# Kernel tuning notes

Hardware: AMD Instinct MI355X
Metric: run time of the kernel (lower is better)

The kernel has to match this reference:

```python
import jax, jax.numpy as jnp
import numpy as np

K_STEPS = 10
ALPHA = 0.1


def setup_inputs() -> dict:
    key = jax.random.key(0)
    k0, k1, k2, k3 = jax.random.split(key, 4)
    N, E, C_IN, C_HID, C_OUT = 100000, 3200000, 512, 256, 64
    x = jax.random.normal(k0, (N, C_IN), dtype=jnp.float32)
    edge_index = jax.random.randint(k1, (2, E), 0, N, dtype=jnp.int64)
    W1 = jax.random.normal(k2, (C_IN, C_HID), dtype=jnp.float32) * (1.0 / np.sqrt(C_IN))
    b1 = jnp.zeros((C_HID,), dtype=jnp.float32)
    W2 = jax.random.normal(k3, (C_HID, C_OUT), dtype=jnp.float32) * (1.0 / np.sqrt(C_HID))
    b2 = jnp.zeros((C_OUT,), dtype=jnp.float32)
    return {"x": x, "edge_index": edge_index, "W1": W1, "b1": b1, "W2": W2, "b2": b2}


def reference(x, edge_index, W1, b1, W2, b2):
    N = x.shape[0]
    src, dst = edge_index[0], edge_index[1]
    # add self-loops (PyG APPNP default)
    loop = jnp.arange(N, dtype=src.dtype)
    src = jnp.concatenate([src, loop])
    dst = jnp.concatenate([dst, loop])
    # GCN symmetric normalization: D^{-1/2} A D^{-1/2}
    deg = jax.ops.segment_sum(jnp.ones_like(dst, dtype=x.dtype), dst, num_segments=N)
    dinv = jnp.where(deg > 0, deg ** -0.5, jnp.zeros_like(deg))
    norm = dinv[src] * dinv[dst]  # [E+N]
    # MLP (dropout is identity at inference)
    h = jax.nn.relu(x @ W1 + b1) @ W2 + b2  # [N, C_OUT]
    # K-step APPNP propagation with teleport
    out = h
    for _ in range(K_STEPS):
        msg = norm[:, None] * out[src]  # [E+N, C_OUT]
        agg = jax.ops.segment_sum(msg, dst, num_segments=N)
        out = (1.0 - ALPHA) * agg + ALPHA * h
    return jax.nn.log_softmax(out, axis=1)
```

## Files before the change

### kernel.cpp

```cpp
#include <hip/hip_runtime.h>
#include <hip/hip_bf16.h>

#define C_IN  512
#define C_HID 256
#define C_OUT 64
#define K_STEPS 10
#define ALPHA 0.1f

#define BKT_SHIFT 9
#define BKT_NODES 512
#define BCAP 24576
#define EPB 4096

typedef _Float16 half8 __attribute__((ext_vector_type(8)));
typedef float f32x4 __attribute__((ext_vector_type(4)));


__global__ __launch_bounds__(256) void k_bucketA(
    const int* __restrict__ src, const int* __restrict__ dst, int E,
    int* __restrict__ bcursor, long long* __restrict__ bedges, int nbkt)
{
    __shared__ int lcount[256];
    __shared__ int lbase[256];
    int t = threadIdx.x;
    int base = blockIdx.x * EPB;
    for (int i = t; i < nbkt; i += 256) lcount[i] = 0;
    __syncthreads();

    int       mybkt[16];
    int       myoff[16];
    long long mypk[16];
    #pragma unroll
    for (int j = 0; j < 16; j++) {
        int e = base + j * 256 + t;
        if (e < E) {
            int s = src[e], d = dst[e];
            int b = d >> BKT_SHIFT;
            mybkt[j] = b;
            mypk[j]  = ((long long)d << 32) | (unsigned int)s;
            myoff[j] = atomicAdd(&lcount[b], 1);
        } else {
            mybkt[j] = -1;
        }
    }
    __syncthreads();
    for (int i = t; i < nbkt; i += 256)
        lbase[i] = lcount[i] ? atomicAdd(&bcursor[i], lcount[i]) : 0;
    __syncthreads();
    #pragma unroll
    for (int j = 0; j < 16; j++) {
        if (mybkt[j] >= 0) {
            int p = lbase[mybkt[j]] + myoff[j];
            bedges[(size_t)mybkt[j] * BCAP + p] = mypk[j];
        }
    }
}

__global__ __launch_bounds__(256) void k_bcount(
    const int* __restrict__ bcursor, const long long* __restrict__ bedges,
    int* __restrict__ counts, int N)
{
    __shared__ int lcnt[BKT_NODES];
    int b = blockIdx.x, t = threadIdx.x;
    int nodebase = b << BKT_SHIFT;
    for (int i = t; i < BKT_NODES; i += 256) lcnt[i] = 0;
    __syncthreads();
    int cnt = bcursor[b];
    const long long* be = bedges + (size_t)b * BCAP;
    for (int i = t; i < cnt; i += 256) {
        int d = (int)(be[i] >> 32);
        atomicAdd(&lcnt[d - nodebase], 1);
    }
    __syncthreads();
    for (int i = t; i < BKT_NODES; i += 256) {
        int node = nodebase + i;
        if (node < N) counts[node] = lcnt[i];
    }
}

__global__ __launch_bounds__(256) void k_bscatter(
    const int* __restrict__ bcursor, const long long* __restrict__ bedges,
    const int* __restrict__ rowptr, int* __restrict__ csr_src, int N)
{
    __shared__ int lcur[BKT_NODES];
    int b = blockIdx.x, t = threadIdx.x;
    int nodebase = b << BKT_SHIFT;
    for (int i = t; i < BKT_NODES; i += 256) {
        int node = nodebase + i;
        lcur[i] = (node < N) ? rowptr[node] : 0;
    }
    __syncthreads();
    int cnt = bcursor[b];
    const long long* be = bedges + (size_t)b * BCAP;
    for (int i = t; i < cnt; i += 256) {
        long long pk = be[i];
        int d = (int)(pk >> 32);
        int s = (int)pk;
        int p = atomicAdd(&lcur[d - nodebase], 1);
        csr_src[p] = s;
    }
}


__global__ void k_dinv(const int* __restrict__ counts, float* __restrict__ dinv, int N) {
    int i = blockIdx.x * blockDim.x + threadIdx.x;
    if (i < N) {
        float deg = (float)(counts[i] + 1);
        dinv[i] = 1.0f / sqrtf(deg);
    }
}

#define SCAN_CHUNK 2048

__global__ void k_scan1(const int* __restrict__ counts, int N, int* __restrict__ bsum) {
    __shared__ int sdata[256];
    int b = blockIdx.x, t = threadIdx.x;
    int base = b * SCAN_CHUNK;
    int sum = 0;
    for (int i = t; i < SCAN_CHUNK; i += 256) {
        int idx = base + i;
        sum += (idx < N) ? counts[idx] : 0;
    }
    sdata[t] = sum;
    __syncthreads();
    for (int off = 128; off; off >>= 1) {
        if (t < off) sdata[t] += sdata[t + off];
        __syncthreads();
    }
    if (t == 0) bsum[b] = sdata[0];
}

__global__ void k_scan2(int* __restrict__ bsum, int nb, int E, int* __restrict__ rowptr, int N) {
    if (blockIdx.x == 0 && threadIdx.x == 0) {
        int run = 0;
        for (int i = 0; i < nb; i++) { int v = bsum[i]; bsum[i] = run; run += v; }
        rowptr[N] = E;
    }
}

__global__ void k_scan3(const int* __restrict__ counts, int N,
                        const int* __restrict__ bsum, int* __restrict__ rowptr) {
    __shared__ int sdata[256];
    int b = blockIdx.x, t = threadIdx.x;
    int base = b * SCAN_CHUNK;
    int vals[8];
    int local = 0;
    #pragma unroll
    for (int i = 0; i < 8; i++) {
        int idx = base + t * 8 + i;
        vals[i] = (idx < N) ? counts[idx] : 0;
        local += vals[i];
    }
    sdata[t] = local;
    __syncthreads();
    for (int off = 1; off < 256; off <<= 1) {
        int y = 0;
        if (t >= off) y = sdata[t - off];
        __syncthreads();
        sdata[t] += y;
        __syncthreads();
    }
    int excl = (t == 0) ? 0 : sdata[t - 1];
    int run = bsum[b] + excl;
    #pragma unroll
    for (int i = 0; i < 8; i++) {
        int idx = base + t * 8 + i;
        if (idx < N) rowptr[idx] = run;
        run += vals[i];
    }
}


__global__ void k_w1t(const float* __restrict__ W, _Float16* __restrict__ Wt) {
    int i = blockIdx.x * 256 + threadIdx.x;
    int k = i >> 8, n = i & 255;
    Wt[(size_t)n * 512 + k] = (_Float16)W[i];
}

__global__ void k_w2t(const float* __restrict__ W, _Float16* __restrict__ Wt) {
    int i = blockIdx.x * 256 + threadIdx.x;
    int k = i >> 6, n = i & 63;
    Wt[(size_t)n * 256 + k] = (_Float16)W[i];
}


__global__ __launch_bounds__(128, 2) void k_mlp1(
    const float* __restrict__ A, const _Float16* __restrict__ Bt,
    const float* __restrict__ bias, _Float16* __restrict__ C, int M)
{
    __shared__ float lds[3][64 * 32];

    int t    = threadIdx.x;
    int lane = t & 63;
    int wc   = t >> 6;
    int bm   = blockIdx.x * 64;
    int mrow = lane & 15;
    int kg   = lane >> 4;

    int srow = t >> 3;
    int cgs  = (t & 7) ^ ((t >> 3) & 7);

    const float* gsrc[4];
    #pragma unroll
    for (int q = 0; q < 4; q++) {
        int gr = bm + q * 16 + srow;
        if (gr >= M) gr = M - 1;
        gsrc[q] = A + (size_t)gr * 512 + cgs * 4;
    }

    #define STAGE(buf, ks)                                                       \
        {                                                                        \
            _Pragma("unroll")                                                    \
            for (int q = 0; q < 4; q++) {                                        \
                __builtin_amdgcn_global_load_lds(                                \
                    (const __attribute__((address_space(1))) void*)(gsrc[q] + (ks) * 32), \
                    (__attribute__((address_space(3))) void*)((char*)&lds[buf][0] + q * 2048 + t * 16), \
                    16, 0, 0);                                                   \
            }                                                                    \
        }

    f32x4 acc[4][8] = {};

    int m7 = lane & 7;
    int rbase[4];
    #pragma unroll
    for (int mi = 0; mi < 4; mi++)
        rbase[mi] = (mi * 16 + mrow) * 32;
    int p0 = ((2 * kg) ^ m7) * 4;
    int p1 = ((2 * kg + 1) ^ m7) * 4;

    STAGE(0, 0);
    STAGE(1, 1);

    #pragma unroll
    for (int ks = 0; ks < 16; ks++) {
        asm volatile("s_waitcnt vmcnt(4) lgkmcnt(0)" ::: "memory");
        __builtin_amdgcn_s_barrier();

        half8 b[8];
        #pragma unroll
        for (int ni = 0; ni < 8; ni++) {
            int n = wc * 128 + ni * 16 + mrow;
            b[ni] = *(const half8*)(Bt + (size_t)n * 512 + ks * 32 + kg * 8);
        }

        if (ks < 14) STAGE((ks + 2) % 3, ks + 2);

        const float* lbuf = &lds[ks % 3][0];

        half8 a[4];
        #pragma unroll
        for (int mi = 0; mi < 4; mi++) {
            f32x4 lo = *(const f32x4*)&lbuf[rbase[mi] + p0];
            f32x4 hi = *(const f32x4*)&lbuf[rbase[mi] + p1];
            a[mi][0] = (_Float16)lo[0]; a[mi][1] = (_Float16)lo[1];
            a[mi][2] = (_Float16)lo[2]; a[mi][3] = (_Float16)lo[3];
            a[mi][4] = (_Float16)hi[0]; a[mi][5] = (_Float16)hi[1];
            a[mi][6] = (_Float16)hi[2]; a[mi][7] = (_Float16)hi[3];
        }

        #pragma unroll
        for (int mi = 0; mi < 4; mi++)
            #pragma unroll
            for (int ni = 0; ni < 8; ni++)
                acc[mi][ni] = __builtin_amdgcn_mfma_f32_16x16x32_f16(
                    a[mi], b[ni], acc[mi][ni], 0, 0, 0);
    }
    #undef STAGE

    #pragma unroll
    for (int mi = 0; mi < 4; mi++) {
        #pragma unroll
        for (int ni = 0; ni < 8; ni++) {
            int n = wc * 128 + ni * 16 + mrow;
            float bv = bias[n];
            #pragma unroll
            for (int rg = 0; rg < 4; rg++) {
                int row = bm + mi * 16 + kg * 4 + rg;
                if (row < M) {
                    float v = acc[mi][ni][rg] + bv;
                    C[(size_t)row * 256 + n] = (_Float16)fmaxf(v, 0.f);
                }
            }
        }
    }
}


__global__ __launch_bounds__(256) void k_mlp2(
    const _Float16* __restrict__ A, const _Float16* __restrict__ Bt,
    const float* __restrict__ bias, const float* __restrict__ dinv,
    _Float16* __restrict__ C, _Float16* __restrict__ Y, int M)
{
    int lane = threadIdx.x & 63;
    int wid  = threadIdx.x >> 6;
    int bm   = blockIdx.x * 256 + wid * 64;
    int mrow = lane & 15;
    int kg   = lane >> 4;
    f32x4 acc[4][4] = {};

    int r[4];
    #pragma unroll
    for (int mi = 0; mi < 4; mi++) {
        int rr = bm + mi * 16 + mrow;
        r[mi] = rr < M ? rr : M - 1;
    }

    for (int k0 = 0; k0 < 256; k0 += 32) {
        int k = k0 + kg * 8;
        half8 a[4], b[4];
        #pragma unroll
        for (int mi = 0; mi < 4; mi++)
            a[mi] = *(const half8*)(A + (size_t)r[mi] * 256 + k);
        #pragma unroll
        for (int ni = 0; ni < 4; ni++) {
            int n = ni * 16 + mrow;
            b[ni] = *(const half8*)(Bt + (size_t)n * 256 + k);
        }
        #pragma unroll
        for (int mi = 0; mi < 4; mi++)
            #pragma unroll
            for (int ni = 0; ni < 4; ni++)
                acc[mi][ni] = __builtin_amdgcn_mfma_f32_16x16x32_f16(
                    a[mi], b[ni], acc[mi][ni], 0, 0, 0);
    }

    #pragma unroll
    for (int mi = 0; mi < 4; mi++) {
        #pragma unroll
        for (int ni = 0; ni < 4; ni++) {
            int n = ni * 16 + mrow;
            float bv = bias[n];
            #pragma unroll
            for (int rg = 0; rg < 4; rg++) {
                int row = bm + mi * 16 + kg * 4 + rg;
                if (row < M) {
                    float v = acc[mi][ni][rg] + bv;
                    C[(size_t)row * 64 + n] = (_Float16)v;
                    Y[(size_t)row * 64 + n] = (_Float16)(v * dinv[row]);
                }
            }
        }
    }
}


template <bool LAST>
__global__ __launch_bounds__(256) void k_prop(
    const int* __restrict__ rowptr, const int* __restrict__ csr_src,
    const float* __restrict__ dinv, const _Float16* __restrict__ h,
    const _Float16* __restrict__ ycur, _Float16* __restrict__ ynxt,
    float* __restrict__ out, int N)
{
    int node = blockIdx.x * 4 + (threadIdx.x >> 6);
    if (node >= N) return;
    int lane = threadIdx.x & 63;
    int g  = lane >> 3;
    int cg = lane & 7;

    int beg = rowptr[node], end = rowptr[node + 1];
    float dn = dinv[node];
    half8 ys = *(const half8*)(ycur + ((size_t)node << 6) + cg * 8);
    half8 hv = *(const half8*)(h    + ((size_t)node << 6) + cg * 8);

    float acc[8] = {};
    for (int e = beg + g; e < end; e += 32) {
        int i1 = e + 8, i2 = e + 16, i3 = e + 24;
        float p1 = (i1 < end) ? 1.f : 0.f;
        float p2 = (i2 < end) ? 1.f : 0.f;
        float p3 = (i3 < end) ? 1.f : 0.f;
        int s0 = csr_src[e];
        int s1 = csr_src[(i1 < end) ? i1 : e];
        int s2 = csr_src[(i2 < end) ? i2 : e];
        int s3 = csr_src[(i3 < end) ? i3 : e];
        half8 v0 = *(const half8*)(ycur + ((size_t)s0 << 6) + cg * 8);
        half8 v1 = *(const half8*)(ycur + ((size_t)s1 << 6) + cg * 8);
        half8 v2 = *(const half8*)(ycur + ((size_t)s2 << 6) + cg * 8);
        half8 v3 = *(const half8*)(ycur + ((size_t)s3 << 6) + cg * 8);
        #pragma unroll
        for (int c = 0; c < 8; c++)
            acc[c] += ((float)v0[c] + p1 * (float)v1[c])
                    + (p2 * (float)v2[c] + p3 * (float)v3[c]);
    }

    #pragma unroll
    for (int c = 0; c < 8; c++) {
        float a = acc[c];
        a += __shfl_xor(a, 8);
        a += __shfl_xor(a, 16);
        a += __shfl_xor(a, 32);
        acc[c] = a;
    }

    float o[8];
    #pragma unroll
    for (int c = 0; c < 8; c++)
        o[c] = (1.0f - ALPHA) * dn * (acc[c] + (float)ys[c]) + ALPHA * (float)hv[c];

    if (!LAST) {
        if (g == 0) {
            half8 w;
            #pragma unroll
            for (int c = 0; c < 8; c++) w[c] = (_Float16)(dn * o[c]);
            *(half8*)(ynxt + ((size_t)node << 6) + cg * 8) = w;
        }
    } else {
        float m = o[0];
        #pragma unroll
        for (int c = 1; c < 8; c++) m = fmaxf(m, o[c]);
        m = fmaxf(m, __shfl_xor(m, 1));
        m = fmaxf(m, __shfl_xor(m, 2));
        m = fmaxf(m, __shfl_xor(m, 4));
        float s = 0.f;
        #pragma unroll
        for (int c = 0; c < 8; c++) s += __expf(o[c] - m);
        s += __shfl_xor(s, 1);
        s += __shfl_xor(s, 2);
        s += __shfl_xor(s, 4);
        float ls = m + logf(s);
        if (g == 0) {
            f32x4 w0, w1;
            #pragma unroll
            for (int c = 0; c < 4; c++) { w0[c] = o[c] - ls; w1[c] = o[c + 4] - ls; }
            float* p = out + ((size_t)node << 6) + cg * 8;
            *(f32x4*)p = w0;
            *(f32x4*)(p + 4) = w1;
        }
    }
}


extern "C" void kernel_launch(void* const* d_in, const int* in_sizes, int n_in,
                              void* d_out, int out_size, void* d_ws, size_t ws_size,
                              hipStream_t stream) {
    const float* x  = (const float*)d_in[0];
    const int*   ei = (const int*)d_in[1];
    const float* W1 = (const float*)d_in[2];
    const float* b1 = (const float*)d_in[3];
    const float* W2 = (const float*)d_in[4];
    const float* b2 = (const float*)d_in[5];

    const int N = in_sizes[0] / C_IN;
    const int E = in_sizes[1] / 2;
    const int* src = ei;
    const int* dst = ei + E;

    char* ws = (char*)d_ws;
    size_t off = 0;
    auto alloc = [&](size_t bytes) -> void* {
        void* p = ws + off;
        off += (bytes + 255) & ~(size_t)255;
        return p;
    };

    int nb   = (N + SCAN_CHUNK - 1) / SCAN_CHUNK;
    int nbkt = (N + BKT_NODES - 1) / BKT_NODES;

    int*       counts  = (int*)      alloc((size_t)4 * N);
    int*       rowptr  = (int*)      alloc((size_t)4 * (N + 1));
    float*     dinv    = (float*)    alloc((size_t)4 * N);
    int*       bsum    = (int*)      alloc((size_t)4 * (nb + 1));
    int*       bcursor = (int*)      alloc((size_t)4 * nbkt);
    int*       csr_src = (int*)      alloc((size_t)4 * E);
    _Float16*  W1t     = (_Float16*) alloc((size_t)2 * C_IN * C_HID);
    _Float16*  W2t     = (_Float16*) alloc((size_t)2 * C_HID * C_OUT);
    _Float16*  hmid    = (_Float16*) alloc((size_t)2 * N * C_HID);
    _Float16*  h       = (_Float16*) alloc((size_t)2 * N * C_OUT);
    _Float16*  ybuf0   = (_Float16*) alloc((size_t)2 * N * C_OUT);
    _Float16*  ybuf1   = (_Float16*) alloc((size_t)2 * N * C_OUT);
    _Float16*  ybuf2   = (_Float16*) alloc((size_t)2 * N * C_OUT);

    long long* bedges = (long long*)hmid;

    hipMemsetAsync(bcursor, 0, (size_t)4 * nbkt, stream);
    k_bucketA<<<(E + EPB - 1) / EPB, 256, 0, stream>>>(src, dst, E, bcursor, bedges, nbkt);
    k_bcount<<<nbkt, 256, 0, stream>>>(bcursor, bedges, counts, N);
    k_dinv<<<(N + 255) / 256, 256, 0, stream>>>(counts, dinv, N);
    k_scan1<<<nb, 256, 0, stream>>>(counts, N, bsum);
    k_scan2<<<1, 64, 0, stream>>>(bsum, nb, E, rowptr, N);
    k_scan3<<<nb, 256, 0, stream>>>(counts, N, bsum, rowptr);
    k_bscatter<<<nbkt, 256, 0, stream>>>(bcursor, bedges, rowptr, csr_src, N);

    k_w1t<<<(C_IN * C_HID) / 256, 256, 0, stream>>>(W1, W1t);
    k_w2t<<<(C_HID * C_OUT) / 256, 256, 0, stream>>>(W2, W2t);
    k_mlp1<<<(N + 63) / 64, 128, 0, stream>>>(x, W1t, b1, hmid, N);
    k_mlp2<<<(N + 255) / 256, 256, 0, stream>>>(hmid, W2t, b2, dinv, h, ybuf0, N);

    int pgrid = (N + 3) / 4;
    _Float16* ycur = ybuf0;
    for (int it = 0; it < K_STEPS - 1; ++it) {
        _Float16* ynxt = (it & 1) ? ybuf2 : ybuf1;
        k_prop<false><<<pgrid, 256, 0, stream>>>(rowptr, csr_src, dinv, h, ycur, ynxt, nullptr, N);
        ycur = ynxt;
    }
    k_prop<true><<<pgrid, 256, 0, stream>>>(rowptr, csr_src, dinv, h, ycur, nullptr, (float*)d_out, N);
}
```

Baseline: 773.3 us.

## Preload full fp16 A tile into LDS once instead of triple-buffered fp32 staging

The k_mlp1 GEMM replaces the triple-buffered async global_load_lds pipeline of fp32 K-slices with a single up-front load of the whole 64x512 row tile. The tile is converted to fp16 and written to 64KB of dynamic LDS with an XOR swizzle, and the main loop then runs with no per-step barriers or conversions. This removes the repeated fp32-to-fp16 conversion and per-iteration synchronisation. In exchange, memory loads no longer overlap with MFMA work inside a block, and the 64KB LDS footprint may limit how many blocks fit on each CU.

```diff
diff --git a/kernel.cpp b/kernel.cpp
--- a/kernel.cpp
+++ b/kernel.cpp
@@ -188,7 +188,7 @@
     const float* __restrict__ A, const _Float16* __restrict__ Bt,
     const float* __restrict__ bias, _Float16* __restrict__ C, int M)
 {
-    __shared__ float lds[3][64 * 32];
+    extern __shared__ __align__(16) _Float16 atile[];
 
     int t    = threadIdx.x;
     int lane = t & 63;
@@ -197,68 +197,41 @@
     int mrow = lane & 15;
     int kg   = lane >> 4;
 
-    int srow = t >> 3;
-    int cgs  = (t & 7) ^ ((t >> 3) & 7);
-
-    const float* gsrc[4];
-    #pragma unroll
-    for (int q = 0; q < 4; q++) {
-        int gr = bm + q * 16 + srow;
+    #pragma unroll
+    for (int j = 0; j < 32; j++) {
+        int chunk = j * 128 + t;
+        int r = chunk >> 6;
+        int c = chunk & 63;
+        int gr = bm + r;
         if (gr >= M) gr = M - 1;
-        gsrc[q] = A + (size_t)gr * 512 + cgs * 4;
-    }
-
-    #define STAGE(buf, ks)                                                       \
-        {                                                                        \
-            _Pragma("unroll")                                                    \
-            for (int q = 0; q < 4; q++) {                                        \
-                __builtin_amdgcn_global_load_lds(                                \
-                    (const __attribute__((address_space(1))) void*)(gsrc[q] + (ks) * 32), \
-                    (__attribute__((address_space(3))) void*)((char*)&lds[buf][0] + q * 2048 + t * 16), \
-                    16, 0, 0);                                                   \
-            }                                                                    \
-        }
+        const float* p = A + (size_t)gr * 512 + c * 8;
+        float4 lo = *(const float4*)p;
+        float4 hi = *(const float4*)(p + 4);
+        half8 v;
+        v[0] = (_Float16)lo.x; v[1] = (_Float16)lo.y;
+        v[2] = (_Float16)lo.z; v[3] = (_Float16)lo.w;
+        v[4] = (_Float16)hi.x; v[5] = (_Float16)hi.y;
+        v[6] = (_Float16)hi.z; v[7] = (_Float16)hi.w;
+        int cs = c ^ (r & 7);
+        *(half8*)&atile[(size_t)r * 512 + cs * 8] = v;
+    }
+    __syncthreads();
 
     f32x4 acc[4][8] = {};
-
-    int m7 = lane & 7;
-    int rbase[4];
-    #pragma unroll
-    for (int mi = 0; mi < 4; mi++)
-        rbase[mi] = (mi * 16 + mrow) * 32;
-    int p0 = ((2 * kg) ^ m7) * 4;
-    int p1 = ((2 * kg + 1) ^ m7) * 4;
-
-    STAGE(0, 0);
-    STAGE(1, 1);
-
-    #pragma unroll
     for (int ks = 0; ks < 16; ks++) {
-        asm volatile("s_waitcnt vmcnt(4) lgkmcnt(0)" ::: "memory");
-        __builtin_amdgcn_s_barrier();
-
         half8 b[8];
         #pragma unroll
         for (int ni = 0; ni < 8; ni++) {
             int n = wc * 128 + ni * 16 + mrow;
             b[ni] = *(const half8*)(Bt + (size_t)n * 512 + ks * 32 + kg * 8);
         }
-
-        if (ks < 14) STAGE((ks + 2) % 3, ks + 2);
-
-        const float* lbuf = &lds[ks % 3][0];
-
         half8 a[4];
         #pragma unroll
         for (int mi = 0; mi < 4; mi++) {
-            f32x4 lo = *(const f32x4*)&lbuf[rbase[mi] + p0];
-            f32x4 hi = *(const f32x4*)&lbuf[rbase[mi] + p1];
-            a[mi][0] = (_Float16)lo[0]; a[mi][1] = (_Float16)lo[1];
-            a[mi][2] = (_Float16)lo[2]; a[mi][3] = (_Float16)lo[3];
-            a[mi][4] = (_Float16)hi[0]; a[mi][5] = (_Float16)hi[1];
-            a[mi][6] = (_Float16)hi[2]; a[mi][7] = (_Float16)hi[3];
-        }
-
+            int r = mi * 16 + mrow;
+            int c = ks * 4 + kg;
+            a[mi] = *(const half8*)&atile[(size_t)r * 512 + (c ^ (r & 7)) * 8];
+        }
         #pragma unroll
         for (int mi = 0; mi < 4; mi++)
             #pragma unroll
@@ -266,7 +239,6 @@
                 acc[mi][ni] = __builtin_amdgcn_mfma_f32_16x16x32_f16(
                     a[mi], b[ni], acc[mi][ni], 0, 0, 0);
     }
-    #undef STAGE
 
     #pragma unroll
     for (int mi = 0; mi < 4; mi++) {
@@ -483,7 +455,7 @@
 
     k_w1t<<<(C_IN * C_HID) / 256, 256, 0, stream>>>(W1, W1t);
     k_w2t<<<(C_HID * C_OUT) / 256, 256, 0, stream>>>(W2, W2t);
-    k_mlp1<<<(N + 63) / 64, 128, 0, stream>>>(x, W1t, b1, hmid, N);
+    k_mlp1<<<(N + 63) / 64, 128, 65536, stream>>>(x, W1t, b1, hmid, N);
     k_mlp2<<<(N + 255) / 256, 256, 0, stream>>>(hmid, W2t, b2, dinv, h, ybuf0, N);
 
     int pgrid = (N + 3) / 4;
```

Measured after the change: 797.2 us. 3.1% more time.

## Retile MLP1 to single-wave 32-row blocks and fold dinv into bcount

Applied to the files above, without the earlier changes.

The first MLP GEMM now runs one 64-lane wave per block over a 32x256 tile instead of two waves over 64x256. Because the wave owns its whole LDS tile, the per-step barrier and lgkmcnt wait are dropped, and it now keeps 32 accumulators. The trade is twice as many B-fragment global loads per A row, higher register pressure and more blocks. Separately, the dinv computation is fused into k_bcount, which removes one kernel launch and one reread of counts.

```diff
diff --git a/kernel.cpp b/kernel.cpp
--- a/kernel.cpp
+++ b/kernel.cpp
@@ -58,7 +58,7 @@
 
 __global__ __launch_bounds__(256) void k_bcount(
     const int* __restrict__ bcursor, const long long* __restrict__ bedges,
-    int* __restrict__ counts, int N)
+    int* __restrict__ counts, float* __restrict__ dinv, int N)
 {
     __shared__ int lcnt[BKT_NODES];
     int b = blockIdx.x, t = threadIdx.x;
@@ -74,7 +74,11 @@
     __syncthreads();
     for (int i = t; i < BKT_NODES; i += 256) {
         int node = nodebase + i;
-        if (node < N) counts[node] = lcnt[i];
+        if (node < N) {
+            int c = lcnt[i];
+            counts[node] = c;
+            dinv[node] = 1.0f / sqrtf((float)(c + 1));
+        }
     }
 }
 
@@ -102,14 +106,6 @@
 }
 
 
-__global__ void k_dinv(const int* __restrict__ counts, float* __restrict__ dinv, int N) {
-    int i = blockIdx.x * blockDim.x + threadIdx.x;
-    if (i < N) {
-        float deg = (float)(counts[i] + 1);
-        dinv[i] = 1.0f / sqrtf(deg);
-    }
-}
-
 #define SCAN_CHUNK 2048
 
 __global__ void k_scan1(const int* __restrict__ counts, int N, int* __restrict__ bsum) {
@@ -184,28 +180,25 @@
 }
 
 
-__global__ __launch_bounds__(128, 2) void k_mlp1(
+__global__ __launch_bounds__(64, 2) void k_mlp1(
     const float* __restrict__ A, const _Float16* __restrict__ Bt,
     const float* __restrict__ bias, _Float16* __restrict__ C, int M)
 {
-    __shared__ float lds[3][64 * 32];
-
-    int t    = threadIdx.x;
-    int lane = t & 63;
-    int wc   = t >> 6;
-    int bm   = blockIdx.x * 64;
+    __shared__ float lds[3][32 * 32];
+
+    int lane = threadIdx.x;
+    int bm   = blockIdx.x * 32;
     int mrow = lane & 15;
     int kg   = lane >> 4;
 
-    int srow = t >> 3;
-    int cgs  = (t & 7) ^ ((t >> 3) & 7);
-
+    int sr = lane >> 3;
+    int sc = (lane & 7) ^ sr;
     const float* gsrc[4];
     #pragma unroll
     for (int q = 0; q < 4; q++) {
-        int gr = bm + q * 16 + srow;
+        int gr = bm + q * 8 + sr;
         if (gr >= M) gr = M - 1;
-        gsrc[q] = A + (size_t)gr * 512 + cgs * 4;
+        gsrc[q] = A + (size_t)gr * 512 + sc * 4;
     }
 
     #define STAGE(buf, ks)                                                       \
@@ -214,45 +207,44 @@
             for (int q = 0; q < 4; q++) {                                        \
                 __builtin_amdgcn_global_load_lds(                                \
                     (const __attribute__((address_space(1))) void*)(gsrc[q] + (ks) * 32), \
-                    (__attribute__((address_space(3))) void*)((char*)&lds[buf][0] + q * 2048 + t * 16), \
+                    (__attribute__((address_space(3))) void*)((char*)&lds[buf][0] + q * 1024 + lane * 16), \
                     16, 0, 0);                                                   \
             }                                                                    \
         }
 
-    f32x4 acc[4][8] = {};
-
-    int m7 = lane & 7;
-    int rbase[4];
-    #pragma unroll
-    for (int mi = 0; mi < 4; mi++)
-        rbase[mi] = (mi * 16 + mrow) * 32;
-    int p0 = ((2 * kg) ^ m7) * 4;
-    int p1 = ((2 * kg + 1) ^ m7) * 4;
+    f32x4 acc[2][16] = {};
+
+    int rbase[2], p0[2], p1[2];
+    #pragma unroll
+    for (int mi = 0; mi < 2; mi++) {
+        int r = mi * 16 + mrow;
+        rbase[mi] = r * 32;
+        p0[mi] = ((2 * kg) ^ (r & 7)) * 4;
+        p1[mi] = ((2 * kg + 1) ^ (r & 7)) * 4;
+    }
 
     STAGE(0, 0);
     STAGE(1, 1);
 
     #pragma unroll
     for (int ks = 0; ks < 16; ks++) {
-        asm volatile("s_waitcnt vmcnt(4) lgkmcnt(0)" ::: "memory");
-        __builtin_amdgcn_s_barrier();
-
-        half8 b[8];
-        #pragma unroll
-        for (int ni = 0; ni < 8; ni++) {
-            int n = wc * 128 + ni * 16 + mrow;
+        asm volatile("s_waitcnt vmcnt(4)" ::: "memory");
+
+        half8 b[16];
+        #pragma unroll
+        for (int ni = 0; ni < 16; ni++) {
+            int n = ni * 16 + mrow;
             b[ni] = *(const half8*)(Bt + (size_t)n * 512 + ks * 32 + kg * 8);
         }
 
         if (ks < 14) STAGE((ks + 2) % 3, ks + 2);
 
         const float* lbuf = &lds[ks % 3][0];
-
-        half8 a[4];
-        #pragma unroll
-        for (int mi = 0; mi < 4; mi++) {
-            f32x4 lo = *(const f32x4*)&lbuf[rbase[mi] + p0];
-            f32x4 hi = *(const f32x4*)&lbuf[rbase[mi] + p1];
+        half8 a[2];
+        #pragma unroll
+        for (int mi = 0; mi < 2; mi++) {
+            f32x4 lo = *(const f32x4*)&lbuf[rbase[mi] + p0[mi]];
+            f32x4 hi = *(const f32x4*)&lbuf[rbase[mi] + p1[mi]];
             a[mi][0] = (_Float16)lo[0]; a[mi][1] = (_Float16)lo[1];
             a[mi][2] = (_Float16)lo[2]; a[mi][3] = (_Float16)lo[3];
             a[mi][4] = (_Float16)hi[0]; a[mi][5] = (_Float16)hi[1];
@@ -260,19 +252,19 @@
         }
 
         #pragma unroll
-        for (int mi = 0; mi < 4; mi++)
-            #pragma unroll
-            for (int ni = 0; ni < 8; ni++)
+        for (int mi = 0; mi < 2; mi++)
+            #pragma unroll
+            for (int ni = 0; ni < 16; ni++)
                 acc[mi][ni] = __builtin_amdgcn_mfma_f32_16x16x32_f16(
                     a[mi], b[ni], acc[mi][ni], 0, 0, 0);
     }
     #undef STAGE
 
     #pragma unroll
-    for (int mi = 0; mi < 4; mi++) {
-        #pragma unroll
-        for (int ni = 0; ni < 8; ni++) {
-            int n = wc * 128 + ni * 16 + mrow;
+    for (int mi = 0; mi < 2; mi++) {
+        #pragma unroll
+        for (int ni = 0; ni < 16; ni++) {
+            int n = ni * 16 + mrow;
             float bv = bias[n];
             #pragma unroll
             for (int rg = 0; rg < 4; rg++) {
@@ -474,8 +466,7 @@
 
     hipMemsetAsync(bcursor, 0, (size_t)4 * nbkt, stream);
     k_bucketA<<<(E + EPB - 1) / EPB, 256, 0, stream>>>(src, dst, E, bcursor, bedges, nbkt);
-    k_bcount<<<nbkt, 256, 0, stream>>>(bcursor, bedges, counts, N);
-    k_dinv<<<(N + 255) / 256, 256, 0, stream>>>(counts, dinv, N);
+    k_bcount<<<nbkt, 256, 0, stream>>>(bcursor, bedges, counts, dinv, N);
     k_scan1<<<nb, 256, 0, stream>>>(counts, N, bsum);
     k_scan2<<<1, 64, 0, stream>>>(bsum, nb, E, rowptr, N);
     k_scan3<<<nb, 256, 0, stream>>>(counts, N, bsum, rowptr);
@@ -483,7 +474,7 @@
 
     k_w1t<<<(C_IN * C_HID) / 256, 256, 0, stream>>>(W1, W1t);
     k_w2t<<<(C_HID * C_OUT) / 256, 256, 0, stream>>>(W2, W2t);
-    k_mlp1<<<(N + 63) / 64, 128, 0, stream>>>(x, W1t, b1, hmid, N);
+    k_mlp1<<<(N + 31) / 32, 64, 0, stream>>>(x, W1t, b1, hmid, N);
     k_mlp2<<<(N + 255) / 256, 256, 0, stream>>>(hmid, W2t, b2, dinv, h, ybuf0, N);
 
     int pgrid = (N + 3) / 4;
```

Measured after the change: 845.1 us. 1.09x slower.
